# Performance work log

Measured on AMD Instinct MI355X. Metric: run time of the kernel, lower is better.

The kernel has to match this reference:

```python
import jax, jax.numpy as jnp
import numpy as np

B, S, C = 32, 128, 32
VOCAB, E, H = 262, 128, 256


def _gru_dir(x_proj, mask, W_hh, b_hh, reverse):
    # x_proj: [C, N, 3H] time-major precomputed input projection
    # mask:   [C, N, 1]  1.0 where char is valid
    N = x_proj.shape[1]
    h0 = jnp.zeros((N, H), x_proj.dtype)

    def step(h, inp):
        x3, mt = inp
        gh = h @ W_hh.T + b_hh                      # [N, 3H]
        hr, hz, hn = jnp.split(gh, 3, axis=-1)
        xr, xz, xn = jnp.split(x3, 3, axis=-1)
        r = jax.nn.sigmoid(xr + hr)
        z = jax.nn.sigmoid(xz + hz)
        n = jnp.tanh(xn + r * hn)
        hnew = (1.0 - z) * n + z * h
        h = mt * hnew + (1.0 - mt) * h              # freeze state past seq end
        return h, None

    hT, _ = jax.lax.scan(step, h0, (x_proj, mask), reverse=reverse)
    return hT  # [N, H] final state at last valid step (fw) / step 0 (bw)


def char_rnn_forward(chars, chars_mask, data_mask, embed,
                     W_ih_fw, W_hh_fw, b_ih_fw, b_hh_fw,
                     W_ih_bw, W_hh_bw, b_ih_bw, b_hh_bw):
    b, s, c = chars.shape
    N = b * s
    x = embed[chars.reshape(N, c)]                      # [N, C, E]
    m = chars_mask.reshape(N, c).astype(x.dtype)        # [N, C]
    mm = jnp.moveaxis(m, 1, 0)[:, :, None]              # [C, N, 1]

    def run(W_ih, b_ih, W_hh, b_hh, reverse):
        xp = jnp.einsum('nce,ge->ncg', x, W_ih) + b_ih  # [N, C, 3H]
        xp = jnp.moveaxis(xp, 1, 0)                     # [C, N, 3H]
        return _gru_dir(xp, mm, W_hh, b_hh, reverse)

    h_fw = run(W_ih_fw, b_ih_fw, W_hh_fw, b_hh_fw, False)
    h_bw = run(W_ih_bw, b_ih_bw, W_hh_bw, b_hh_bw, True)
    final = jnp.concatenate([h_fw, h_bw], axis=-1).reshape(b, s, 2 * H)
    return final * data_mask[:, :, None].astype(final.dtype)


def setup_inputs() -> dict:
    key = jax.random.key(0)
    ks = jax.random.split(key, 16)
    chars = jax.random.randint(ks[0], (B, S, C), 0, VOCAB, dtype=jnp.int32)
    # ragged but contiguous lengths, as pack_padded_sequence assumes (>=1)
    word_len = jax.random.randint(ks[1], (B,), 1, S + 1)
    char_len = jax.random.randint(ks[2], (B, S), 1, C + 1)
    data_mask = (jnp.arange(S)[None, :] < word_len[:, None]).astype(jnp.int32)
    chars_mask = (jnp.arange(C)[None, None, :] < char_len[:, :, None]).astype(jnp.int32)
    chars_mask = chars_mask * data_mask[:, :, None]
    # pack_padded needs length>=1 even for padded words (torch never runs them;
    # we mask their output with data_mask, so give them 1 valid char)
    chars_mask = chars_mask.at[:, :, 0].set(1)

    sc = 1.0 / np.sqrt(H)
    def unif(k, shape):
        return jax.random.uniform(k, shape, jnp.float32, -sc, sc)
    embed = jax.random.normal(ks[3], (VOCAB, E), jnp.float32) * 0.1
    return {
        'chars': chars, 'chars_mask': chars_mask, 'data_mask': data_mask,
        'embed': embed,
        'W_ih_fw': unif(ks[4], (3 * H, E)), 'W_hh_fw': unif(ks[5], (3 * H, H)),
        'b_ih_fw': unif(ks[6], (3 * H,)),  'b_hh_fw': unif(ks[7], (3 * H,)),
        'W_ih_bw': unif(ks[8], (3 * H, E)), 'W_hh_bw': unif(ks[9], (3 * H, H)),
        'b_ih_bw': unif(ks[10], (3 * H,)), 'b_hh_bw': unif(ks[11], (3 * H,)),
    }


def reference(chars, chars_mask, data_mask, embed,
              W_ih_fw, W_hh_fw, b_ih_fw, b_hh_fw,
              W_ih_bw, W_hh_bw, b_ih_bw, b_hh_bw):
    return char_rnn_forward(chars, chars_mask, data_mask, embed,
                            W_ih_fw, W_hh_fw, b_ih_fw, b_hh_fw,
                            W_ih_bw, W_hh_bw, b_ih_bw, b_hh_bw)
```

## Files before the change

kernel.cpp:

```cpp
#include <hip/hip_runtime.h>
#include <hip/hip_bf16.h>

typedef unsigned int u32;
typedef unsigned short u16;
typedef __attribute__((ext_vector_type(8))) short bf16x8;
typedef __attribute__((ext_vector_type(4))) float f32x4;

#define NWORDS 4096
#define CC 32
#define EE 128
#define HHH 256
#define MMW 32
#define VOCABN 262

#define HS 272
#define XPS 784

#define PK_HHD (16*3*8*512)
#define XP_OFF_U16 (2*PK_HHD)
#define XPD (VOCABN*768)
#define BIAS_OFF_U16 (XP_OFF_U16 + 2*XPD)

__device__ __forceinline__ float bf2f(u16 u){ union{u32 i; float f;} v; v.i=((u32)u)<<16; return v.f; }
__device__ __forceinline__ u16 f2bf(float f){
  __hip_bfloat16 h = __float2bfloat16(f);
  u16 r; __builtin_memcpy(&r, &h, 2); return r;
}
__device__ __forceinline__ float sigmoid_f(float x){
  float e = __builtin_amdgcn_exp2f(-1.4426950408889634f * x);
  return __builtin_amdgcn_rcpf(1.0f + e);
}
__device__ __forceinline__ float tanh_f(float x){
  float ax = __builtin_fabsf(x);
  float e  = __builtin_amdgcn_exp2f(-2.8853900817779268f * ax);
  float t  = 1.0f - 2.0f * e * __builtin_amdgcn_rcpf(1.0f + e);
  return __builtin_copysignf(t, x);
}

__global__ void prep_pack(const float* __restrict__ Whh_fw, const float* __restrict__ Whh_bw,
                          u16* __restrict__ wsu)
{
  int idx = blockIdx.x*256 + threadIdx.x;
  int d = idx / PK_HHD;
  int e = idx - d*PK_HHD;
  const float* Whh = d ? Whh_bw : Whh_fw;
  int jj   = e & 7;
  int lane = (e >> 3) & 63;
  int kc   = (e >> 9) & 7;
  int gnt  = e >> 12;
  int g = gnt % 3, nt = gnt / 3;
  int row = g*256 + nt*16 + (lane & 15);
  int k   = kc*32 + ((lane >> 4) << 3) + jj;
  wsu[idx] = f2bf(Whh[row*HHH + k]);
}

#define XP_NCH 8
#define XP_CBLK ((VOCABN + XP_NCH - 1) / XP_NCH)
__global__ void prep_xp(const float* __restrict__ emb,
                        const float* __restrict__ Wih_fw, const float* __restrict__ Wih_bw,
                        u16* __restrict__ wsu)
{
  const int dirb = blockIdx.x & 1;
  const int c0   = (blockIdx.x >> 1) * XP_NCH;
  const int t    = threadIdx.x;
  const float* Wih = dirb ? Wih_bw : Wih_fw;
  u16* xpo = wsu + XP_OFF_U16 + (size_t)dirb*XPD;

  __shared__ float sh_E[XP_NCH][EE];
  for (int i = t; i < XP_NCH*EE; i += 256) {
    int c = c0 + i/EE;
    sh_E[0][i] = (c < VOCABN) ? emb[(size_t)c*EE + (i & (EE-1))] : 0.0f;
  }
  __syncthreads();

  #pragma unroll 1
  for (int q = 0; q < 3; ++q) {
    const int g = q*256 + t;
    const float* W = Wih + (size_t)g*EE;
    float acc[XP_NCH];
    #pragma unroll
    for (int c = 0; c < XP_NCH; ++c) acc[c] = 0.0f;
    #pragma unroll 2
    for (int k = 0; k < EE; k += 4) {
      float4 wv = *(const float4*)(W + k);
      #pragma unroll
      for (int c = 0; c < XP_NCH; ++c) {
        float4 ev = *(const float4*)(&sh_E[c][k]);
        acc[c] = fmaf(ev.w, wv.w, fmaf(ev.z, wv.z, fmaf(ev.y, wv.y, fmaf(ev.x, wv.x, acc[c]))));
      }
    }
    #pragma unroll
    for (int c = 0; c < XP_NCH; ++c) {
      int ci = c0 + c;
      if (ci < VOCABN) xpo[(size_t)ci*768 + g] = f2bf(acc[c]);
    }
  }
}

__global__ void prep_bias(const float* __restrict__ bih_fw, const float* __restrict__ bhh_fw,
                          const float* __restrict__ bih_bw, const float* __restrict__ bhh_bw,
                          u16* __restrict__ wsu)
{
  int i = blockIdx.x*256 + threadIdx.x;
  if (i >= 2048) return;
  int d = i >> 10, o = i & 1023;
  const float* bih = d ? bih_bw : bih_fw;
  const float* bhh = d ? bhh_bw : bhh_fw;
  float v;
  if (o < 512)      v = bih[o] + bhh[o];
  else if (o < 768) v = bih[o - 512 + 512];
  else              v = bhh[o - 768 + 512];
  ((float*)(wsu + BIAS_OFF_U16))[d*1024 + o] = v;
}

__global__ __launch_bounds__(1024)
void gru_mfma(const int* __restrict__ chars, const int* __restrict__ chars_mask,
              const int* __restrict__ data_mask, const u16* __restrict__ wsu,
              float* __restrict__ out)
{
  const int dir   = blockIdx.x & 1;
  const int word0 = (blockIdx.x >> 1) * MMW;
  const int j     = threadIdx.x;
  const int wave  = j >> 6, lane = j & 63;
  const int quad  = lane >> 4, l15 = lane & 15;

  const bf16x8* pHH  = (const bf16x8*)(wsu + (size_t)dir*PK_HHD);
  const u16*    xpt  = wsu + XP_OFF_U16 + (size_t)dir*XPD;
  const float*  bias = (const float*)(wsu + BIAS_OFF_U16) + dir*1024;

  const bf16x8* bHH = pHH + (size_t)(wave*3)*8*64 + lane;

  __shared__ __align__(16) u16   sh_hhi[MMW][HS];
  __shared__ __align__(16) u16   sh_hlo[MMW][HS];
  __shared__ __align__(16) u16   sh_xp[MMW][XPS];
  __shared__ float sh_m[MMW];

  for (int i = j; i < MMW*HS/2; i += 1024) { ((float*)sh_hhi)[i] = 0.0f; ((float*)sh_hlo)[i] = 0.0f; }

  const int ch = wave*16 + l15;
  const float bR  = bias[ch],        bZ  = bias[256 + ch];
  const float bXN = bias[512 + ch],  bHN = bias[768 + ch];

  const int sw = j >> 5, sp = j & 31;

  bf16x8 buf[4][3];
  auto load_batch = [&](int kc, bf16x8 dst[3]) {
    #pragma unroll
    for (int g = 0; g < 3; ++g) dst[g] = bHH[(g*8 + kc)*64];
  };
  load_batch(0, buf[0]);
  load_batch(1, buf[1]);
  load_batch(2, buf[2]);

  #pragma unroll 1
  for (int s = 0; s < CC; ++s) {
    const int t = dir ? (CC - 1 - s) : s;
    __syncthreads();
    {
      int ci = chars[(word0 + sw)*CC + t];
      const uint4* src = (const uint4*)(xpt + (size_t)ci*768);
      uint4 a0 = src[sp*3], a1 = src[sp*3+1], a2 = src[sp*3+2];
      *(uint4*)&sh_xp[sw][sp*24]      = a0;
      *(uint4*)&sh_xp[sw][sp*24 + 8]  = a1;
      *(uint4*)&sh_xp[sw][sp*24 + 16] = a2;
      if (j < MMW) sh_m[j] = (float)chars_mask[(word0 + j)*CC + t];
    }
    __syncthreads();

    f32x4 acc[3][2];
    #pragma unroll
    for (int m = 0; m < 2; ++m) {
      acc[0][m] = (f32x4){bR,bR,bR,bR};
      acc[1][m] = (f32x4){bZ,bZ,bZ,bZ};
      acc[2][m] = (f32x4){bHN,bHN,bHN,bHN};
    }

    auto mfma_batch = [&](int kc, bf16x8 src[3]) {
      #pragma unroll
      for (int m = 0; m < 2; ++m) {
        bf16x8 ah = *(const bf16x8*)&sh_hhi[m*16 + l15][kc*32 + quad*8];
        bf16x8 al = *(const bf16x8*)&sh_hlo[m*16 + l15][kc*32 + quad*8];
        #pragma unroll
        for (int g = 0; g < 3; ++g) {
          const int ai = (g < 2) ? g : 2;
          acc[ai][m] = __builtin_amdgcn_mfma_f32_16x16x32_bf16(ah, src[g], acc[ai][m], 0,0,0);
          acc[ai][m] = __builtin_amdgcn_mfma_f32_16x16x32_bf16(al, src[g], acc[ai][m], 0,0,0);
        }
      }
    };

    #pragma unroll
    for (int b = 0; b < 8; ++b) {
      mfma_batch(b, buf[b & 3]);
      load_batch((b + 3) & 7, buf[(b + 3) & 3]);
    }

    __syncthreads();

    #pragma unroll
    for (int m = 0; m < 2; ++m)
      #pragma unroll
      for (int r = 0; r < 4; ++r) {
        const int word = m*16 + quad*4 + r;
        float xr = bf2f(sh_xp[word][ch]);
        float xz = bf2f(sh_xp[word][256 + ch]);
        float xn = bf2f(sh_xp[word][512 + ch]);
        float rr = sigmoid_f(acc[0][m][r] + xr);
        float zz = sigmoid_f(acc[1][m][r] + xz);
        float nn = tanh_f(fmaf(rr, acc[2][m][r], bXN + xn));
        float hold = bf2f(sh_hhi[word][ch]) + bf2f(sh_hlo[word][ch]);
        float hnew = fmaf(zz, hold - nn, nn);
        float hm   = fmaf(sh_m[word], hnew - hold, hold);
        u16 hi = f2bf(hm);
        sh_hhi[word][ch] = hi;
        sh_hlo[word][ch] = f2bf(hm - bf2f(hi));
      }
  }
  __syncthreads();

  const int oc = j & 255, og = j >> 8;
  #pragma unroll
  for (int i = 0; i < 8; ++i) {
    const int w = og*8 + i;
    float dm = (float)data_mask[word0 + w];
    float h = bf2f(sh_hhi[w][oc]) + bf2f(sh_hlo[w][oc]);
    out[(size_t)(word0 + w)*(2*HHH) + dir*HHH + oc] = h * dm;
  }
}

extern "C" void kernel_launch(void* const* d_in, const int* in_sizes, int n_in,
                              void* d_out, int out_size, void* d_ws, size_t ws_size,
                              hipStream_t stream) {
  const int*   chars      = (const int*)d_in[0];
  const int*   chars_mask = (const int*)d_in[1];
  const int*   data_mask  = (const int*)d_in[2];
  const float* embed      = (const float*)d_in[3];
  const float* Wih_fw     = (const float*)d_in[4];
  const float* Whh_fw     = (const float*)d_in[5];
  const float* bih_fw     = (const float*)d_in[6];
  const float* bhh_fw     = (const float*)d_in[7];
  const float* Wih_bw     = (const float*)d_in[8];
  const float* Whh_bw     = (const float*)d_in[9];
  const float* bih_bw     = (const float*)d_in[10];
  const float* bhh_bw     = (const float*)d_in[11];
  u16* wsu = (u16*)d_ws;

  prep_pack<<<2*PK_HHD/256, 256, 0, stream>>>(Whh_fw, Whh_bw, wsu);
  prep_xp<<<XP_CBLK*2, 256, 0, stream>>>(embed, Wih_fw, Wih_bw, wsu);
  prep_bias<<<8, 256, 0, stream>>>(bih_fw, bhh_fw, bih_bw, bhh_bw, wsu);

  gru_mfma<<<(NWORDS/MMW)*2, 1024, 0, stream>>>(chars, chars_mask, data_mask, wsu, (float*)d_out);
}
```

Baseline: 427.6 us.

## Merge prep kernels, preload chars/masks to LDS, drop low-part MFMAs for r/z gates

The three prep kernels become one launch that dispatches on block index, removing two kernel launches. The GRU kernel loads all char indices and masks for its words into shared memory once, instead of reading global memory at every step. The hidden-state low-part MFMAs are skipped for the r and z gates (kept only for n), cutting MFMA count from 6 to 4 per batch, with a small precision loss on those gates. The hidden-state LDS row stride shrinks from 272 to 264, which changes bank mapping.

```diff
diff --git a/kernel.cpp b/kernel.cpp
--- a/kernel.cpp
+++ b/kernel.cpp
@@ -13,13 +13,19 @@
 #define MMW 32
 #define VOCABN 262
 
-#define HS 272
+#define HS 264
 #define XPS 784
 
 #define PK_HHD (16*3*8*512)
 #define XP_OFF_U16 (2*PK_HHD)
 #define XPD (VOCABN*768)
 #define BIAS_OFF_U16 (XP_OFF_U16 + 2*XPD)
+
+#define XP_NCH 8
+#define XP_CBLK ((VOCABN + XP_NCH - 1) / XP_NCH)
+#define PREP_PACK_BLKS (2*PK_HHD/256)
+#define PREP_XP_BLKS (XP_CBLK*2)
+#define PREP_BLKS (PREP_PACK_BLKS + PREP_XP_BLKS + 1)
 
 __device__ __forceinline__ float bf2f(u16 u){ union{u32 i; float f;} v; v.i=((u32)u)<<16; return v.f; }
 __device__ __forceinline__ u16 f2bf(float f){
@@ -37,80 +43,77 @@
   return __builtin_copysignf(t, x);
 }
 
-__global__ void prep_pack(const float* __restrict__ Whh_fw, const float* __restrict__ Whh_bw,
-                          u16* __restrict__ wsu)
+__global__ void prep_all(const float* __restrict__ emb,
+                         const float* __restrict__ Wih_fw, const float* __restrict__ Whh_fw,
+                         const float* __restrict__ bih_fw, const float* __restrict__ bhh_fw,
+                         const float* __restrict__ Wih_bw, const float* __restrict__ Whh_bw,
+                         const float* __restrict__ bih_bw, const float* __restrict__ bhh_bw,
+                         u16* __restrict__ wsu)
 {
-  int idx = blockIdx.x*256 + threadIdx.x;
-  int d = idx / PK_HHD;
-  int e = idx - d*PK_HHD;
-  const float* Whh = d ? Whh_bw : Whh_fw;
-  int jj   = e & 7;
-  int lane = (e >> 3) & 63;
-  int kc   = (e >> 9) & 7;
-  int gnt  = e >> 12;
-  int g = gnt % 3, nt = gnt / 3;
-  int row = g*256 + nt*16 + (lane & 15);
-  int k   = kc*32 + ((lane >> 4) << 3) + jj;
-  wsu[idx] = f2bf(Whh[row*HHH + k]);
-}
-
-#define XP_NCH 8
-#define XP_CBLK ((VOCABN + XP_NCH - 1) / XP_NCH)
-__global__ void prep_xp(const float* __restrict__ emb,
-                        const float* __restrict__ Wih_fw, const float* __restrict__ Wih_bw,
-                        u16* __restrict__ wsu)
-{
-  const int dirb = blockIdx.x & 1;
-  const int c0   = (blockIdx.x >> 1) * XP_NCH;
-  const int t    = threadIdx.x;
-  const float* Wih = dirb ? Wih_bw : Wih_fw;
-  u16* xpo = wsu + XP_OFF_U16 + (size_t)dirb*XPD;
-
-  __shared__ float sh_E[XP_NCH][EE];
-  for (int i = t; i < XP_NCH*EE; i += 256) {
-    int c = c0 + i/EE;
-    sh_E[0][i] = (c < VOCABN) ? emb[(size_t)c*EE + (i & (EE-1))] : 0.0f;
-  }
-  __syncthreads();
-
-  #pragma unroll 1
-  for (int q = 0; q < 3; ++q) {
-    const int g = q*256 + t;
-    const float* W = Wih + (size_t)g*EE;
-    float acc[XP_NCH];
-    #pragma unroll
-    for (int c = 0; c < XP_NCH; ++c) acc[c] = 0.0f;
-    #pragma unroll 2
-    for (int k = 0; k < EE; k += 4) {
-      float4 wv = *(const float4*)(W + k);
+  const int bid = blockIdx.x, tid = threadIdx.x;
+  if (bid < PREP_PACK_BLKS) {
+    int idx = bid*256 + tid;
+    int d = idx / PK_HHD;
+    int e = idx - d*PK_HHD;
+    const float* Whh = d ? Whh_bw : Whh_fw;
+    int jj   = e & 7;
+    int lane = (e >> 3) & 63;
+    int kc   = (e >> 9) & 7;
+    int gnt  = e >> 12;
+    int g = gnt % 3, nt = gnt / 3;
+    int row = g*256 + nt*16 + (lane & 15);
+    int k   = kc*32 + ((lane >> 4) << 3) + jj;
+    wsu[idx] = f2bf(Whh[row*HHH + k]);
+  } else if (bid < PREP_PACK_BLKS + PREP_XP_BLKS) {
+    const int b    = bid - PREP_PACK_BLKS;
+    const int dirb = b & 1;
+    const int c0   = (b >> 1) * XP_NCH;
+    const float* Wih = dirb ? Wih_bw : Wih_fw;
+    u16* xpo = wsu + XP_OFF_U16 + (size_t)dirb*XPD;
+
+    __shared__ float sh_E[XP_NCH][EE];
+    for (int i = tid; i < XP_NCH*EE; i += 256) {
+      int c = c0 + i/EE;
+      sh_E[0][i] = (c < VOCABN) ? emb[(size_t)c*EE + (i & (EE-1))] : 0.0f;
+    }
+    __syncthreads();
+
+    #pragma unroll 1
+    for (int q = 0; q < 3; ++q) {
+      const int g = q*256 + tid;
+      const float* W = Wih + (size_t)g*EE;
+      float acc[XP_NCH];
+      #pragma unroll
+      for (int c = 0; c < XP_NCH; ++c) acc[c] = 0.0f;
+      #pragma unroll 2
+      for (int k = 0; k < EE; k += 4) {
+        float4 wv = *(const float4*)(W + k);
+        #pragma unroll
+        for (int c = 0; c < XP_NCH; ++c) {
+          float4 ev = *(const float4*)(&sh_E[c][k]);
+          acc[c] = fmaf(ev.w, wv.w, fmaf(ev.z, wv.z, fmaf(ev.y, wv.y, fmaf(ev.x, wv.x, acc[c]))));
+        }
+      }
       #pragma unroll
       for (int c = 0; c < XP_NCH; ++c) {
-        float4 ev = *(const float4*)(&sh_E[c][k]);
-        acc[c] = fmaf(ev.w, wv.w, fmaf(ev.z, wv.z, fmaf(ev.y, wv.y, fmaf(ev.x, wv.x, acc[c]))));
-      }
-    }
-    #pragma unroll
-    for (int c = 0; c < XP_NCH; ++c) {
-      int ci = c0 + c;
-      if (ci < VOCABN) xpo[(size_t)ci*768 + g] = f2bf(acc[c]);
-    }
-  }
-}
-
-__global__ void prep_bias(const float* __restrict__ bih_fw, const float* __restrict__ bhh_fw,
-                          const float* __restrict__ bih_bw, const float* __restrict__ bhh_bw,
-                          u16* __restrict__ wsu)
-{
-  int i = blockIdx.x*256 + threadIdx.x;
-  if (i >= 2048) return;
-  int d = i >> 10, o = i & 1023;
-  const float* bih = d ? bih_bw : bih_fw;
-  const float* bhh = d ? bhh_bw : bhh_fw;
-  float v;
-  if (o < 512)      v = bih[o] + bhh[o];
-  else if (o < 768) v = bih[o - 512 + 512];
-  else              v = bhh[o - 768 + 512];
-  ((float*)(wsu + BIAS_OFF_U16))[d*1024 + o] = v;
+        int ci = c0 + c;
+        if (ci < VOCABN) xpo[(size_t)ci*768 + g] = f2bf(acc[c]);
+      }
+    }
+  } else {
+    #pragma unroll
+    for (int rep = 0; rep < 8; ++rep) {
+      int i = rep*256 + tid;
+      int d = i >> 10, o = i & 1023;
+      const float* bih = d ? bih_bw : bih_fw;
+      const float* bhh = d ? bhh_bw : bhh_fw;
+      float v;
+      if (o < 512)      v = bih[o] + bhh[o];
+      else if (o < 768) v = bih[o - 512 + 512];
+      else              v = bhh[o - 768 + 512];
+      ((float*)(wsu + BIAS_OFF_U16))[d*1024 + o] = v;
+    }
+  }
 }
 
 __global__ __launch_bounds__(1024)
@@ -133,8 +136,14 @@
   __shared__ __align__(16) u16   sh_hhi[MMW][HS];
   __shared__ __align__(16) u16   sh_hlo[MMW][HS];
   __shared__ __align__(16) u16   sh_xp[MMW][XPS];
-  __shared__ float sh_m[MMW];
-
+  __shared__ int   sh_ci[MMW][CC + 1];
+  __shared__ float sh_cm[MMW][CC + 1];
+
+  {
+    const int w = j >> 5, c = j & 31;
+    sh_ci[w][c] = chars[(word0 + w)*CC + c];
+    sh_cm[w][c] = (float)chars_mask[(word0 + w)*CC + c];
+  }
   for (int i = j; i < MMW*HS/2; i += 1024) { ((float*)sh_hhi)[i] = 0.0f; ((float*)sh_hlo)[i] = 0.0f; }
 
   const int ch = wave*16 + l15;
@@ -157,13 +166,12 @@
     const int t = dir ? (CC - 1 - s) : s;
     __syncthreads();
     {
-      int ci = chars[(word0 + sw)*CC + t];
+      int ci = sh_ci[sw][t];
       const uint4* src = (const uint4*)(xpt + (size_t)ci*768);
       uint4 a0 = src[sp*3], a1 = src[sp*3+1], a2 = src[sp*3+2];
       *(uint4*)&sh_xp[sw][sp*24]      = a0;
       *(uint4*)&sh_xp[sw][sp*24 + 8]  = a1;
       *(uint4*)&sh_xp[sw][sp*24 + 16] = a2;
-      if (j < MMW) sh_m[j] = (float)chars_mask[(word0 + j)*CC + t];
     }
     __syncthreads();
 
@@ -180,12 +188,10 @@
       for (int m = 0; m < 2; ++m) {
         bf16x8 ah = *(const bf16x8*)&sh_hhi[m*16 + l15][kc*32 + quad*8];
         bf16x8 al = *(const bf16x8*)&sh_hlo[m*16 + l15][kc*32 + quad*8];
-        #pragma unroll
-        for (int g = 0; g < 3; ++g) {
-          const int ai = (g < 2) ? g : 2;
-          acc[ai][m] = __builtin_amdgcn_mfma_f32_16x16x32_bf16(ah, src[g], acc[ai][m], 0,0,0);
-          acc[ai][m] = __builtin_amdgcn_mfma_f32_16x16x32_bf16(al, src[g], acc[ai][m], 0,0,0);
-        }
+        acc[0][m] = __builtin_amdgcn_mfma_f32_16x16x32_bf16(ah, src[0], acc[0][m], 0,0,0);
+        acc[1][m] = __builtin_amdgcn_mfma_f32_16x16x32_bf16(ah, src[1], acc[1][m], 0,0,0);
+        acc[2][m] = __builtin_amdgcn_mfma_f32_16x16x32_bf16(ah, src[2], acc[2][m], 0,0,0);
+        acc[2][m] = __builtin_amdgcn_mfma_f32_16x16x32_bf16(al, src[2], acc[2][m], 0,0,0);
       }
     };
 
@@ -210,7 +216,7 @@
         float nn = tanh_f(fmaf(rr, acc[2][m][r], bXN + xn));
         float hold = bf2f(sh_hhi[word][ch]) + bf2f(sh_hlo[word][ch]);
         float hnew = fmaf(zz, hold - nn, nn);
-        float hm   = fmaf(sh_m[word], hnew - hold, hold);
+        float hm   = fmaf(sh_cm[word][t], hnew - hold, hold);
         u16 hi = f2bf(hm);
         sh_hhi[word][ch] = hi;
         sh_hlo[word][ch] = f2bf(hm - bf2f(hi));
@@ -245,9 +251,8 @@
   const float* bhh_bw     = (const float*)d_in[11];
   u16* wsu = (u16*)d_ws;
 
-  prep_pack<<<2*PK_HHD/256, 256, 0, stream>>>(Whh_fw, Whh_bw, wsu);
-  prep_xp<<<XP_CBLK*2, 256, 0, stream>>>(embed, Wih_fw, Wih_bw, wsu);
-  prep_bias<<<8, 256, 0, stream>>>(bih_fw, bhh_fw, bih_bw, bhh_bw, wsu);
+  prep_all<<<PREP_BLKS, 256, 0, stream>>>(embed, Wih_fw, Whh_fw, bih_fw, bhh_fw,
+                                          Wih_bw, Whh_bw, bih_bw, bhh_bw, wsu);
 
   gru_mfma<<<(NWORDS/MMW)*2, 1024, 0, stream>>>(chars, chars_mask, data_mask, wsu, (float*)d_out);
 }
```

Result: faster. 366.3 us, median of 2 (-14.3%).
